# Performance work log

Measured on AMD Instinct MI355X. Metric: run time of the kernel, lower is better.

## Reference

```python
import jax, jax.numpy as jnp
import numpy as np

B, F, N = 8, 64, 256
EPS = 1e-09


def setup_inputs() -> dict:
    key = jax.random.key(0)
    k = jax.random.split(key, 4)
    x = jax.random.normal(k[0], (B, F, N, N), dtype=jnp.float32)
    mask = jax.random.randint(k[1], (B, N), 0, 2).astype(jnp.float32)
    weight = jnp.ones((1, F, 1, 1), dtype=jnp.float32)
    weight_exp = jax.random.normal(k[2], (1, F, 1, 1), dtype=jnp.float32)
    weight_bias = jnp.zeros((1, F, 1, 1), dtype=jnp.float32)
    bias = jax.random.normal(k[3], (1, F, 1), dtype=jnp.float32)
    return dict(x=x, mask=mask, weight=weight, weight_exp=weight_exp,
                weight_bias=weight_bias, bias=bias)


def reference(x, mask, weight, weight_exp, weight_bias, bias):
    # mask: [B, N] -> pairwise mask [B, 1, N, N] (broadcast over features,
    # same math as torch .expand to [B, F, N, N])
    m2 = mask[:, None, :, None] * mask[:, None, None, :]
    mdiag = mask * mask                       # diagonal of pairwise mask, [B, N]
    n = jnp.sum(mdiag, axis=-1, keepdims=True)  # [B, 1] (identical across F)
    n2 = jnp.clip(n - 1.0, 1.0)

    # trace(A * mask) per (b, f)
    diagA = jnp.einsum('bfii->bfi', x)
    trace = jnp.sum(diagA * mdiag[:, None, :], axis=-1)        # [B, F]
    # trace(A^2 * mask): diag(A @ A)_i = sum_k A[i,k] A[k,i]  (O(N^2), same math
    # as torch.linalg.matrix_power(A, 2) followed by masked diagonal trace)
    diagA2 = jnp.einsum('bfik,bfki->bfi', x, x)
    trace_sq = jnp.sum(diagA2 * mdiag[:, None, :], axis=-1)    # [B, F]

    mean = trace / n
    variance = trace_sq / n2 - trace ** 2 / (n * n2)
    mean_b = mean.mean(axis=1)      # [B]
    var_b = variance.mean(axis=1)   # [B]

    eye = jnp.eye(N, dtype=x.dtype)
    m_t = mean_b[:, None, None, None] * eye          # diag_embed of mean
    x_centered = (x - m_t) * m2
    x_norm = x_centered / jnp.sqrt(var_b[:, None, None, None] + EPS)

    bias_diag = bias[..., None] * eye                # [1, F, N, N] diag_embed
    return x_norm * (weight * jnp.exp(weight_exp) + weight_bias) + bias_diag
```

## Files before the change

### kernel.cpp

```cpp
#include <hip/hip_runtime.h>
#include <math.h>

#define BB 8
#define FF 64
#define NN 256
#define EPSF 1e-9f

typedef float floatx4 __attribute__((ext_vector_type(4)));


__device__ __forceinline__ int jit(int half, int e) {
    constexpr int IT0[5] = {0, 1, 0, 0, 0};
    constexpr int IT1[5] = {2, 3, 1, 1, 2};
    return half ? IT1[e] : IT0[e];
}
__device__ __forceinline__ int jkt(int half, int e) {
    constexpr int KT0[5] = {0, 1, 1, 2, 3};
    constexpr int KT1[5] = {2, 3, 2, 3, 3};
    return half ? KT1[e] : KT0[e];
}

__global__ __launch_bounds__(256) void k_traces(const float* __restrict__ x,
                                                const float* __restrict__ mask,
                                                float* __restrict__ ws) {
    __shared__ float md[NN];
    __shared__ float T1[64][65];
    __shared__ float T2[64][65];
    __shared__ float red[4][2];
    const int t    = threadIdx.x;
    const int bh   = blockIdx.x;
    const int bf   = bh >> 1;
    const int half = bh & 1;
    const int b    = bf >> 6;
    const float* __restrict__ xm = x + (size_t)bf * (NN * NN);

    { float m = mask[b * NN + t]; md[t] = m * m; }

    const int lane = t & 63;
    const int w    = t >> 6;
    const int la   = t >> 4;
    const int lc4  = (t & 15) << 2;
    float acc2 = 0.f, trp = 0.f;

    float4 p1[4], p2[4];

    {
        const int i0 = jit(half, 0) << 6, k0 = jkt(half, 0) << 6;
        #pragma unroll
        for (int rr = 0; rr < 4; ++rr) {
            int a = la + (rr << 4);
            p1[rr] = *(const float4*)(xm + (size_t)(i0 + a) * NN + k0 + lc4);
        }
    }

    #pragma unroll
    for (int e = 0; e < 5; ++e) {
        const bool diag = (e < 2);
        const int i0 = jit(half, e) << 6;
        const int k0 = jkt(half, e) << 6;

        #pragma unroll
        for (int rr = 0; rr < 4; ++rr) {
            int a = la + (rr << 4);
            T1[a][lc4 + 0] = p1[rr].x; T1[a][lc4 + 1] = p1[rr].y;
            T1[a][lc4 + 2] = p1[rr].z; T1[a][lc4 + 3] = p1[rr].w;
            if (!diag) {
                T2[a][lc4 + 0] = p2[rr].x; T2[a][lc4 + 1] = p2[rr].y;
                T2[a][lc4 + 2] = p2[rr].z; T2[a][lc4 + 3] = p2[rr].w;
            }
        }
        __syncthreads();

        if (e < 4) {
            const int ni0 = jit(half, e + 1) << 6;
            const int nk0 = jkt(half, e + 1) << 6;
            #pragma unroll
            for (int rr = 0; rr < 4; ++rr) {
                int a = la + (rr << 4);
                p1[rr] = *(const float4*)(xm + (size_t)(ni0 + a) * NN + nk0 + lc4);
                if (e + 1 >= 2)
                    p2[rr] = *(const float4*)(xm + (size_t)(nk0 + a) * NN + ni0 + lc4);
            }
        }

        if (!diag) {
            #pragma unroll
            for (int s = 0; s < 16; ++s) {
                int a = w + (s << 2);
                acc2 += T1[a][lane] * T2[lane][a] * (md[i0 + a] + md[k0 + lane]);
            }
        } else {
            #pragma unroll
            for (int s = 0; s < 16; ++s) {
                int a = w + (s << 2);
                acc2 += T1[a][lane] * T1[lane][a] * md[i0 + a];
                if (lane == a) trp += T1[a][a] * md[i0 + a];
            }
        }
        __syncthreads();
    }

    #pragma unroll
    for (int off = 32; off > 0; off >>= 1) {
        acc2 += __shfl_down(acc2, off);
        trp  += __shfl_down(trp,  off);
    }
    if (lane == 0) { red[w][0] = trp; red[w][1] = acc2; }
    __syncthreads();
    if (t == 0) {
        ws[bh]        = red[0][0] + red[1][0] + red[2][0] + red[3][0];
        ws[1024 + bh] = red[0][1] + red[1][1] + red[2][1] + red[3][1];
    }
}

__global__ __launch_bounds__(256) void k_out(const float* __restrict__ x,
                                             const float* __restrict__ mask,
                                             const float* __restrict__ wt,
                                             const float* __restrict__ wexp,
                                             const float* __restrict__ wbias,
                                             const float* __restrict__ bias,
                                             const float* __restrict__ ws,
                                             float* __restrict__ out) {
    __shared__ float smean[BB], sistd[BB], sg[FF], sb[FF];
    const int t    = threadIdx.x;
    const int lane = t & 63;
    const int w    = t >> 6;

    for (int bb = w; bb < BB; bb += 4) {
        const int base = (bb << 7) + (lane << 1);
        float trf = ws[base] + ws[base + 1];
        float tsf = ws[1024 + base] + ws[1024 + base + 1];
        float tr2 = trf * trf;
        float m0 = mask[(bb << 8) + lane];
        float m1 = mask[(bb << 8) + lane + 64];
        float m2 = mask[(bb << 8) + lane + 128];
        float m3 = mask[(bb << 8) + lane + 192];
        float nn = m0 * m0 + m1 * m1 + m2 * m2 + m3 * m3;
        #pragma unroll
        for (int off = 32; off > 0; off >>= 1) {
            trf += __shfl_down(trf, off);
            tr2 += __shfl_down(tr2, off);
            tsf += __shfl_down(tsf, off);
            nn  += __shfl_down(nn,  off);
        }
        if (lane == 0) {
            float n  = nn;
            float n2 = fmaxf(n - 1.f, 1.f);
            smean[bb] = trf / (64.f * n);
            sistd[bb] = 1.f / sqrtf(tsf / (64.f * n2) - tr2 / (64.f * n * n2) + EPSF);
        }
    }
    if (t < FF) { sg[t] = wt[t] * expf(wexp[t]) + wbias[t]; sb[t] = bias[t]; }
    __syncthreads();

    const int total4 = (BB * FF * NN * NN) >> 2;
    const int stride = gridDim.x * blockDim.x;
    for (int idx4 = blockIdx.x * blockDim.x + t; idx4 < total4; idx4 += stride) {
        int e = idx4 << 2;
        int j = e & (NN - 1);
        int i = (e >> 8) & (NN - 1);
        int f = (e >> 16) & (FF - 1);
        int b = e >> 22;
        float4 xv = ((const float4*)x)[idx4];
        float  mi = mask[(b << 8) + i];
        float4 mj = ((const float4*)mask)[((b << 8) + j) >> 2];
        float meanb   = smean[b];
        float inv_std = sistd[b];
        float g  = sg[f];
        float bs = sb[f];
        float s  = mi * inv_std * g;
        floatx4 o;
        o.x = (xv.x - (i == j     ? meanb : 0.f)) * mj.x * s + (i == j     ? bs : 0.f);
        o.y = (xv.y - (i == j + 1 ? meanb : 0.f)) * mj.y * s + (i == j + 1 ? bs : 0.f);
        o.z = (xv.z - (i == j + 2 ? meanb : 0.f)) * mj.z * s + (i == j + 2 ? bs : 0.f);
        o.w = (xv.w - (i == j + 3 ? meanb : 0.f)) * mj.w * s + (i == j + 3 ? bs : 0.f);
        __builtin_nontemporal_store(o, &((floatx4*)out)[idx4]);
    }
}

extern "C" void kernel_launch(void* const* d_in, const int* in_sizes, int n_in,
                              void* d_out, int out_size, void* d_ws, size_t ws_size,
                              hipStream_t stream) {
    const float* x     = (const float*)d_in[0];
    const float* mask  = (const float*)d_in[1];
    const float* wt    = (const float*)d_in[2];
    const float* wexp  = (const float*)d_in[3];
    const float* wbias = (const float*)d_in[4];
    const float* bias  = (const float*)d_in[5];
    float* out = (float*)d_out;
    float* ws  = (float*)d_ws;

    hipLaunchKernelGGL(k_traces, dim3(BB * FF * 2), dim3(256), 0, stream, x, mask, ws);
    hipLaunchKernelGGL(k_out,    dim3(2048),        dim3(256), 0, stream,
                       x, mask, wt, wexp, wbias, bias, ws, out);
}
```

Before: 65.73 us.

## Fuse trace reduction and normalization into one cooperative kernel with grid sync

Adds a cooperative kernel with one block per (batch, feature) matrix. Each block computes its masked trace and trace-of-square over 10 tile pairs, publishes them, waits on a grid-wide sync, derives the per-batch statistics, and then normalizes and writes its own matrix. The aim is to drop the second kernel launch and have the re-read of each matrix come from cache rather than HBM. In exchange it gives up half the blocks of the trace phase, runs a serial, non-unrolled write loop per block, and adds a grid barrier. The original two-kernel path stays as a fallback with shifted workspace offsets.

```diff
diff --git a/kernel.cpp b/kernel.cpp
--- a/kernel.cpp
+++ b/kernel.cpp
@@ -1,5 +1,8 @@
 #include <hip/hip_runtime.h>
+#include <hip/hip_cooperative_groups.h>
 #include <math.h>
+
+namespace cg = cooperative_groups;
 
 #define BB 8
 #define FF 64
@@ -7,6 +10,154 @@
 #define EPSF 1e-9f
 
 typedef float floatx4 __attribute__((ext_vector_type(4)));
+
+
+__device__ __forceinline__ int fit(int e) {
+    constexpr int IT[10] = {0,1,2,3, 0,0,0,1,1,2};
+    return IT[e];
+}
+__device__ __forceinline__ int fkt(int e) {
+    constexpr int KT[10] = {0,1,2,3, 1,2,3,2,3,3};
+    return KT[e];
+}
+
+__global__ __launch_bounds__(256, 2) void k_fused(
+    const float* __restrict__ x, const float* __restrict__ mask,
+    const float* __restrict__ wt, const float* __restrict__ wexp,
+    const float* __restrict__ wbias, const float* __restrict__ bias,
+    float* __restrict__ out, float* __restrict__ ws) {
+
+    __shared__ float md[NN];
+    __shared__ float T1[64][65];
+    __shared__ float T2[64][65];
+    __shared__ float red[4][2];
+    __shared__ float sstats[4];
+
+    const int t  = threadIdx.x;
+    const int bf = blockIdx.x;
+    const int b  = bf >> 6;
+    const int f  = bf & 63;
+    const float* __restrict__ xm = x + (size_t)bf * (NN * NN);
+
+    { float m = mask[b * NN + t]; md[t] = m * m; }
+
+    const int lane = t & 63;
+    const int w    = t >> 6;
+    const int la   = t >> 4;
+    const int lc4  = (t & 15) << 2;
+    float acc2 = 0.f, trp = 0.f;
+    float4 p1[4], p2[4];
+
+    #pragma unroll
+    for (int rr = 0; rr < 4; ++rr)
+        p1[rr] = *(const float4*)(xm + (size_t)(la + (rr << 4)) * NN + lc4);
+
+    #pragma unroll
+    for (int e = 0; e < 10; ++e) {
+        const bool diag = (e < 4);
+        const int i0 = fit(e) << 6;
+        const int k0 = fkt(e) << 6;
+
+        #pragma unroll
+        for (int rr = 0; rr < 4; ++rr) {
+            int a = la + (rr << 4);
+            T1[a][lc4 + 0] = p1[rr].x; T1[a][lc4 + 1] = p1[rr].y;
+            T1[a][lc4 + 2] = p1[rr].z; T1[a][lc4 + 3] = p1[rr].w;
+            if (!diag) {
+                T2[a][lc4 + 0] = p2[rr].x; T2[a][lc4 + 1] = p2[rr].y;
+                T2[a][lc4 + 2] = p2[rr].z; T2[a][lc4 + 3] = p2[rr].w;
+            }
+        }
+        __syncthreads();
+
+        if (e < 9) {
+            const int ni0 = fit(e + 1) << 6;
+            const int nk0 = fkt(e + 1) << 6;
+            #pragma unroll
+            for (int rr = 0; rr < 4; ++rr) {
+                int a = la + (rr << 4);
+                p1[rr] = *(const float4*)(xm + (size_t)(ni0 + a) * NN + nk0 + lc4);
+                if (e + 1 >= 4)
+                    p2[rr] = *(const float4*)(xm + (size_t)(nk0 + a) * NN + ni0 + lc4);
+            }
+        }
+
+        if (!diag) {
+            #pragma unroll
+            for (int s = 0; s < 16; ++s) {
+                int a = w + (s << 2);
+                acc2 += T1[a][lane] * T2[lane][a] * (md[i0 + a] + md[k0 + lane]);
+            }
+        } else {
+            #pragma unroll
+            for (int s = 0; s < 16; ++s) {
+                int a = w + (s << 2);
+                acc2 += T1[a][lane] * T1[lane][a] * md[i0 + a];
+                if (lane == a) trp += T1[a][a] * md[i0 + a];
+            }
+        }
+        __syncthreads();
+    }
+
+    #pragma unroll
+    for (int off = 32; off > 0; off >>= 1) {
+        acc2 += __shfl_down(acc2, off);
+        trp  += __shfl_down(trp,  off);
+    }
+    if (lane == 0) { red[w][0] = trp; red[w][1] = acc2; }
+    __syncthreads();
+    if (t == 0) {
+        float trace = red[0][0] + red[1][0] + red[2][0] + red[3][0];
+        float tsq   = red[0][1] + red[1][1] + red[2][1] + red[3][1];
+        __hip_atomic_store(&ws[bf],       trace, __ATOMIC_RELAXED, __HIP_MEMORY_SCOPE_AGENT);
+        __hip_atomic_store(&ws[512 + bf], tsq,   __ATOMIC_RELAXED, __HIP_MEMORY_SCOPE_AGENT);
+    }
+
+    cg::this_grid().sync();
+
+    if (w == 0) {
+        float trf = __hip_atomic_load(&ws[(b << 6) + lane],       __ATOMIC_RELAXED, __HIP_MEMORY_SCOPE_AGENT);
+        float tsf = __hip_atomic_load(&ws[512 + (b << 6) + lane], __ATOMIC_RELAXED, __HIP_MEMORY_SCOPE_AGENT);
+        float tr2 = trf * trf;
+        float nn  = md[lane] + md[lane + 64] + md[lane + 128] + md[lane + 192];
+        #pragma unroll
+        for (int off = 32; off > 0; off >>= 1) {
+            trf += __shfl_down(trf, off);
+            tr2 += __shfl_down(tr2, off);
+            tsf += __shfl_down(tsf, off);
+            nn  += __shfl_down(nn,  off);
+        }
+        if (lane == 0) {
+            float n  = nn;
+            float n2 = fmaxf(n - 1.f, 1.f);
+            sstats[0] = trf / (64.f * n);
+            sstats[1] = 1.f / sqrtf(tsf / (64.f * n2) - tr2 / (64.f * n * n2) + EPSF);
+            sstats[2] = wt[f] * expf(wexp[f]) + wbias[f];
+            sstats[3] = bias[f];
+        }
+    }
+    __syncthreads();
+
+    const float meanb = sstats[0];
+    const float istd  = sstats[1];
+    const float g     = sstats[2];
+    const float bsf   = sstats[3];
+    float* __restrict__ om = out + (size_t)bf * (NN * NN);
+
+    for (int it4 = 0; it4 < 64; ++it4) {
+        int idx4 = (it4 << 8) + t;
+        int i  = idx4 >> 6;
+        int j0 = (idx4 & 63) << 2;
+        float4 xv = *(const float4*)(xm + (size_t)i * NN + j0);
+        float s = md[i] * istd * g;
+        floatx4 o;
+        o.x = (xv.x - (i == j0     ? meanb : 0.f)) * md[j0    ] * s + (i == j0     ? bsf : 0.f);
+        o.y = (xv.y - (i == j0 + 1 ? meanb : 0.f)) * md[j0 + 1] * s + (i == j0 + 1 ? bsf : 0.f);
+        o.z = (xv.z - (i == j0 + 2 ? meanb : 0.f)) * md[j0 + 2] * s + (i == j0 + 2 ? bsf : 0.f);
+        o.w = (xv.w - (i == j0 + 3 ? meanb : 0.f)) * md[j0 + 3] * s + (i == j0 + 3 ? bsf : 0.f);
+        __builtin_nontemporal_store(o, (floatx4*)(om + (size_t)i * NN + j0));
+    }
+}
 
 
 __device__ __forceinline__ int jit(int half, int e) {
@@ -41,16 +192,13 @@
     const int la   = t >> 4;
     const int lc4  = (t & 15) << 2;
     float acc2 = 0.f, trp = 0.f;
-
     float4 p1[4], p2[4];
 
     {
         const int i0 = jit(half, 0) << 6, k0 = jkt(half, 0) << 6;
         #pragma unroll
-        for (int rr = 0; rr < 4; ++rr) {
-            int a = la + (rr << 4);
-            p1[rr] = *(const float4*)(xm + (size_t)(i0 + a) * NN + k0 + lc4);
-        }
+        for (int rr = 0; rr < 4; ++rr)
+            p1[rr] = *(const float4*)(xm + (size_t)(i0 + la + (rr << 4)) * NN + k0 + lc4);
     }
 
     #pragma unroll
@@ -58,7 +206,6 @@
         const bool diag = (e < 2);
         const int i0 = jit(half, e) << 6;
         const int k0 = jkt(half, e) << 6;
-
         #pragma unroll
         for (int rr = 0; rr < 4; ++rr) {
             int a = la + (rr << 4);
@@ -70,7 +217,6 @@
             }
         }
         __syncthreads();
-
         if (e < 4) {
             const int ni0 = jit(half, e + 1) << 6;
             const int nk0 = jkt(half, e + 1) << 6;
@@ -82,7 +228,6 @@
                     p2[rr] = *(const float4*)(xm + (size_t)(nk0 + a) * NN + ni0 + lc4);
             }
         }
-
         if (!diag) {
             #pragma unroll
             for (int s = 0; s < 16; ++s) {
@@ -108,8 +253,8 @@
     if (lane == 0) { red[w][0] = trp; red[w][1] = acc2; }
     __syncthreads();
     if (t == 0) {
-        ws[bh]        = red[0][0] + red[1][0] + red[2][0] + red[3][0];
-        ws[1024 + bh] = red[0][1] + red[1][1] + red[2][1] + red[3][1];
+        ws[1024 + bh] = red[0][0] + red[1][0] + red[2][0] + red[3][0];
+        ws[2048 + bh] = red[0][1] + red[1][1] + red[2][1] + red[3][1];
     }
 }
 
@@ -127,7 +272,7 @@
     const int w    = t >> 6;
 
     for (int bb = w; bb < BB; bb += 4) {
-        const int base = (bb << 7) + (lane << 1);
+        const int base = 1024 + (bb << 7) + (lane << 1);
         float trf = ws[base] + ws[base + 1];
         float tsf = ws[1024 + base] + ws[1024 + base + 1];
         float tr2 = trf * trf;
@@ -190,6 +335,23 @@
     float* out = (float*)d_out;
     float* ws  = (float*)d_ws;
 
+    int dev = 0;
+    (void)hipGetDevice(&dev);
+    int nCU = 0;
+    (void)hipDeviceGetAttribute(&nCU, hipDeviceAttributeMultiprocessorCount, dev);
+    int maxb = 0;
+    (void)hipOccupancyMaxActiveBlocksPerMultiprocessor(&maxb, (const void*)k_fused, 256, 0);
+
+    if (maxb > 0 && (long)maxb * (long)nCU >= 512) {
+        void* args[] = {(void*)&x, (void*)&mask, (void*)&wt, (void*)&wexp,
+                        (void*)&wbias, (void*)&bias, (void*)&out, (void*)&ws};
+        if (hipLaunchCooperativeKernel((const void*)k_fused, dim3(512), dim3(256),
+                                       args, 0, stream) == hipSuccess) {
+            return;
+        }
+        (void)hipGetLastError();
+    }
+
     hipLaunchKernelGGL(k_traces, dim3(BB * FF * 2), dim3(256), 0, stream, x, mask, ws);
     hipLaunchKernelGGL(k_out,    dim3(2048),        dim3(256), 0, stream,
                        x, mask, wt, wexp, wbias, bias, ws, out);
```

Result: slower. 126.4 us (+92.4%).

## Split trace kernel into one block per 64x64 tile pair job

Applied to the files above, without the earlier changes.

The trace kernel now launches 512x10 blocks, one per (matrix, tile job), instead of 1024 blocks that each loop over five tile pairs with register prefetch. For off-diagonal jobs, the transposed tile is kept in registers rather than staged in a second shared-memory array. This halves shared memory and adds an occupancy hint, aiming for more parallelism and latency hiding. The cost is more blocks, no intra-block pipelining, and a ten-way partial-sum reduction in the output kernel.

```diff
diff --git a/kernel.cpp b/kernel.cpp
--- a/kernel.cpp
+++ b/kernel.cpp
@@ -9,95 +9,74 @@
 typedef float floatx4 __attribute__((ext_vector_type(4)));
 
 
-__device__ __forceinline__ int jit(int half, int e) {
-    constexpr int IT0[5] = {0, 1, 0, 0, 0};
-    constexpr int IT1[5] = {2, 3, 1, 1, 2};
-    return half ? IT1[e] : IT0[e];
+__device__ __forceinline__ int fit(int e) {
+    constexpr int IT[10] = {0,1,2,3, 0,0,0,1,1,2};
+    return IT[e];
 }
-__device__ __forceinline__ int jkt(int half, int e) {
-    constexpr int KT0[5] = {0, 1, 1, 2, 3};
-    constexpr int KT1[5] = {2, 3, 2, 3, 3};
-    return half ? KT1[e] : KT0[e];
+__device__ __forceinline__ int fkt(int e) {
+    constexpr int KT[10] = {0,1,2,3, 1,2,3,2,3,3};
+    return KT[e];
 }
 
-__global__ __launch_bounds__(256) void k_traces(const float* __restrict__ x,
-                                                const float* __restrict__ mask,
-                                                float* __restrict__ ws) {
-    __shared__ float md[NN];
+__global__ __launch_bounds__(256, 6) void k_traces(const float* __restrict__ x,
+                                                   const float* __restrict__ mask,
+                                                   float* __restrict__ ws) {
     __shared__ float T1[64][65];
-    __shared__ float T2[64][65];
+    __shared__ float mdi[64], mdk[64];
     __shared__ float red[4][2];
-    const int t    = threadIdx.x;
-    const int bh   = blockIdx.x;
-    const int bf   = bh >> 1;
-    const int half = bh & 1;
-    const int b    = bf >> 6;
-    const float* __restrict__ xm = x + (size_t)bf * (NN * NN);
 
-    { float m = mask[b * NN + t]; md[t] = m * m; }
+    const int t   = threadIdx.x;
+    const int mat = blockIdx.x;
+    const int job = blockIdx.y;
+    const int b   = mat >> 6;
+    const int i0  = fit(job) << 6;
+    const int k0  = fkt(job) << 6;
+    const bool diag = (job < 4);
+    const float* __restrict__ xm = x + (size_t)mat * (NN * NN);
 
+    if (t < 64)       { float m = mask[b * NN + i0 + t];      mdi[t]      = m * m; }
+    else if (t < 128) { float m = mask[b * NN + k0 + t - 64]; mdk[t - 64] = m * m; }
+
+    const int la  = t >> 4;
+    const int lc4 = (t & 15) << 2;
     const int lane = t & 63;
     const int w    = t >> 6;
-    const int la   = t >> 4;
-    const int lc4  = (t & 15) << 2;
+
+    float4 p[4];
+    float4 u[4];
+    #pragma unroll
+    for (int rr = 0; rr < 4; ++rr) {
+        const int a = la + (rr << 4);
+        p[rr] = *(const float4*)(xm + (size_t)(i0 + a) * NN + k0 + lc4);
+        if (!diag)
+            u[rr] = *(const float4*)(xm + (size_t)(k0 + a) * NN + i0 + lc4);
+    }
+    #pragma unroll
+    for (int rr = 0; rr < 4; ++rr) {
+        const int a = la + (rr << 4);
+        T1[a][lc4 + 0] = p[rr].x; T1[a][lc4 + 1] = p[rr].y;
+        T1[a][lc4 + 2] = p[rr].z; T1[a][lc4 + 3] = p[rr].w;
+    }
+    __syncthreads();
+
     float acc2 = 0.f, trp = 0.f;
-
-    float4 p1[4], p2[4];
-
-    {
-        const int i0 = jit(half, 0) << 6, k0 = jkt(half, 0) << 6;
+    if (!diag) {
         #pragma unroll
         for (int rr = 0; rr < 4; ++rr) {
-            int a = la + (rr << 4);
-            p1[rr] = *(const float4*)(xm + (size_t)(i0 + a) * NN + k0 + lc4);
+            const int c = la + (rr << 4);
+            const float mk = mdk[c];
+            acc2 += T1[lc4 + 0][c] * u[rr].x * (mdi[lc4 + 0] + mk);
+            acc2 += T1[lc4 + 1][c] * u[rr].y * (mdi[lc4 + 1] + mk);
+            acc2 += T1[lc4 + 2][c] * u[rr].z * (mdi[lc4 + 2] + mk);
+            acc2 += T1[lc4 + 3][c] * u[rr].w * (mdi[lc4 + 3] + mk);
         }
-    }
-
-    #pragma unroll
-    for (int e = 0; e < 5; ++e) {
-        const bool diag = (e < 2);
-        const int i0 = jit(half, e) << 6;
-        const int k0 = jkt(half, e) << 6;
-
+    } else {
         #pragma unroll
-        for (int rr = 0; rr < 4; ++rr) {
-            int a = la + (rr << 4);
-            T1[a][lc4 + 0] = p1[rr].x; T1[a][lc4 + 1] = p1[rr].y;
-            T1[a][lc4 + 2] = p1[rr].z; T1[a][lc4 + 3] = p1[rr].w;
-            if (!diag) {
-                T2[a][lc4 + 0] = p2[rr].x; T2[a][lc4 + 1] = p2[rr].y;
-                T2[a][lc4 + 2] = p2[rr].z; T2[a][lc4 + 3] = p2[rr].w;
-            }
+        for (int s = 0; s < 16; ++s) {
+            const int a = w + (s << 2);
+            acc2 += T1[a][lane] * T1[lane][a] * mdi[a];
+            if (lane == a) trp += T1[a][a] * mdi[a];
         }
-        __syncthreads();
-
-        if (e < 4) {
-            const int ni0 = jit(half, e + 1) << 6;
-            const int nk0 = jkt(half, e + 1) << 6;
-            #pragma unroll
-            for (int rr = 0; rr < 4; ++rr) {
-                int a = la + (rr << 4);
-                p1[rr] = *(const float4*)(xm + (size_t)(ni0 + a) * NN + nk0 + lc4);
-                if (e + 1 >= 2)
-                    p2[rr] = *(const float4*)(xm + (size_t)(nk0 + a) * NN + ni0 + lc4);
-            }
-        }
-
-        if (!diag) {
-            #pragma unroll
-            for (int s = 0; s < 16; ++s) {
-                int a = w + (s << 2);
-                acc2 += T1[a][lane] * T2[lane][a] * (md[i0 + a] + md[k0 + lane]);
-            }
-        } else {
-            #pragma unroll
-            for (int s = 0; s < 16; ++s) {
-                int a = w + (s << 2);
-                acc2 += T1[a][lane] * T1[lane][a] * md[i0 + a];
-                if (lane == a) trp += T1[a][a] * md[i0 + a];
-            }
-        }
-        __syncthreads();
     }
 
     #pragma unroll
@@ -108,8 +87,8 @@
     if (lane == 0) { red[w][0] = trp; red[w][1] = acc2; }
     __syncthreads();
     if (t == 0) {
-        ws[bh]        = red[0][0] + red[1][0] + red[2][0] + red[3][0];
-        ws[1024 + bh] = red[0][1] + red[1][1] + red[2][1] + red[3][1];
+        ws[(mat << 4) + job]        = red[0][0] + red[1][0] + red[2][0] + red[3][0];
+        ws[8192 + (mat << 4) + job] = red[0][1] + red[1][1] + red[2][1] + red[3][1];
     }
 }
 
@@ -127,9 +106,13 @@
     const int w    = t >> 6;
 
     for (int bb = w; bb < BB; bb += 4) {
-        const int base = (bb << 7) + (lane << 1);
-        float trf = ws[base] + ws[base + 1];
-        float tsf = ws[1024 + base] + ws[1024 + base + 1];
+        const int base = ((bb << 6) + lane) << 4;
+        float trf = 0.f, tsf = 0.f;
+        #pragma unroll
+        for (int j = 0; j < 10; ++j) {
+            trf += ws[base + j];
+            tsf += ws[8192 + base + j];
+        }
         float tr2 = trf * trf;
         float m0 = mask[(bb << 8) + lane];
         float m1 = mask[(bb << 8) + lane + 64];
@@ -190,7 +173,7 @@
     float* out = (float*)d_out;
     float* ws  = (float*)d_ws;
 
-    hipLaunchKernelGGL(k_traces, dim3(BB * FF * 2), dim3(256), 0, stream, x, mask, ws);
-    hipLaunchKernelGGL(k_out,    dim3(2048),        dim3(256), 0, stream,
+    hipLaunchKernelGGL(k_traces, dim3(512, 10), dim3(256), 0, stream, x, mask, ws);
+    hipLaunchKernelGGL(k_out,    dim3(2048),    dim3(256), 0, stream,
                        x, mask, wt, wexp, wbias, bias, ws, out);
 }
```

Result: slower. 67.44 us (+2.6%).
